# Kernel optimization log

Hardware: AMD Instinct MI355X
Metric: run time of the kernel (lower is better)

## Reference

```python
import jax, jax.numpy as jnp
import numpy as np

SCALE = 0.1  # FullAttention(0.1) binds scale positionally

def setup_inputs() -> dict:
    key = jax.random.key(0)
    k1, k2, k3, k4, k5 = jax.random.split(key, 5)
    B, H, L, E = 128, 16, 64, 128
    C = H * E  # in_channel = 2048
    return {
        "queries": jax.random.normal(k1, (B, H, L, E), dtype=jnp.float32),
        "keys": jax.random.normal(k2, (B, H, L, E), dtype=jnp.float32),
        "values": jax.random.normal(k3, (B, H, L, E), dtype=jnp.float32),
        "W": jax.random.normal(k4, (C, C), dtype=jnp.float32) * (1.0 / np.sqrt(C)),
        "b": jax.random.normal(k5, (C,), dtype=jnp.float32) * 0.01,
    }

def reference(queries, keys, values, W, b):
    # inputs are [B, H, L, E]; module permutes to [B, L, H, E]
    q = jnp.transpose(queries, (0, 2, 1, 3))  # blhe
    k = jnp.transpose(keys, (0, 2, 1, 3))     # bshe
    v = jnp.transpose(values, (0, 2, 1, 3))   # bshd
    scores = jnp.einsum('blhe,bshe->bhls', q, k)
    A = jax.nn.softmax(SCALE * scores, axis=-1)  # dropout is identity in eval
    V = jnp.einsum('bhls,bshd->blhd', A, v)
    B_, L, H, D = V.shape
    out = V.reshape(-1, 64, H * D)  # view(-1, 64, in_channel)
    return out @ W.T + b
```

## Files before the change

kernel.cpp:

```cpp
#include <hip/hip_runtime.h>
#include <hip/hip_bf16.h>
#include <stdint.h>

typedef __bf16 bf16_t;
typedef __bf16 bf16x4 __attribute__((ext_vector_type(4)));
typedef __bf16 bf16x8 __attribute__((ext_vector_type(8)));
typedef float  f32x4  __attribute__((ext_vector_type(4)));

#define AS1 __attribute__((address_space(1)))
#define AS3 __attribute__((address_space(3)))

__device__ __forceinline__ void gld_lds16(const void* gp, void* lp) {
    __builtin_amdgcn_global_load_lds((const AS1 unsigned int*)gp,
                                     (AS3 unsigned int*)lp, 16, 0, 0);
}

__device__ __forceinline__ bf16_t bhi(float v) { return (bf16_t)v; }
__device__ __forceinline__ bf16_t blo(float v) {
    return (bf16_t)(v - (float)((bf16_t)v));
}

__global__ __launch_bounds__(256) void wconv_kernel(const float* __restrict__ W,
                                                    bf16_t* __restrict__ Wb) {
    const int i = (blockIdx.x * 256 + threadIdx.x) * 4;
    const float4 f = *(const float4*)&W[i];
    bf16x4 v = { (bf16_t)f.x, (bf16_t)f.y, (bf16_t)f.z, (bf16_t)f.w };
    *(bf16x4*)&Wb[i] = v;
}

__global__ __launch_bounds__(256, 3) void attn_kernel(const float* __restrict__ Q,
                                                      const float* __restrict__ K,
                                                      const float* __restrict__ V,
                                                      bf16_t* __restrict__ X) {
    __shared__ __align__(16) char smem[49152];
    bf16_t* KL = (bf16_t*)smem;
    bf16_t* KH = (bf16_t*)(smem + 16384);
    bf16_t* Vt = (bf16_t*)(smem + 32768);
    bf16_t* Ps = (bf16_t*)smem;
    bf16_t* Ob = (bf16_t*)(smem + 16384);

    const int bh    = blockIdx.x;
    const int b     = bh >> 4;
    const int h     = bh & 15;
    const int t     = threadIdx.x;
    const int w     = t >> 6;
    const int lane  = t & 63;
    const int row16 = lane & 15;
    const int quad  = lane >> 4;

    const float* Qg = Q + (size_t)bh * 8192;
    const float* Kg = K + (size_t)bh * 8192;
    const float* Vg = V + (size_t)bh * 8192;

    bf16x8 qh8[4], ql8[4];
    {
        const float* qrow = Qg + (size_t)(16 * w + row16) * 128 + 8 * quad;
#pragma unroll
        for (int kc = 0; kc < 4; ++kc) {
            const float4 f0 = *(const float4*)&qrow[32 * kc];
            const float4 f1 = *(const float4*)&qrow[32 * kc + 4];
            const float f[8] = { f0.x, f0.y, f0.z, f0.w, f1.x, f1.y, f1.z, f1.w };
            bf16x8 hi, lo;
#pragma unroll
            for (int j = 0; j < 8; ++j) {
                const bf16_t hv = (bf16_t)f[j];
                hi[j] = hv;
                lo[j] = (bf16_t)(f[j] - (float)hv);
            }
            qh8[kc] = hi;
            ql8[kc] = lo;
        }
    }

    {
        const int r   = t >> 2;
        const int c0  = (t & 3) * 32;
        const int rsw = r & 7;
#pragma unroll
        for (int j = 0; j < 8; ++j) {
            const int c = c0 + 4 * j;
            const float4 f = *(const float4*)&Kg[r * 128 + c];
            bf16x4 hi = { bhi(f.x), bhi(f.y), bhi(f.z), bhi(f.w) };
            bf16x4 lo = { blo(f.x), blo(f.y), blo(f.z), blo(f.w) };
            const int addr = r * 128 + ((((c >> 3) ^ rsw)) << 3) + (c & 7);
            *(bf16x4*)&KH[addr] = hi;
            *(bf16x4*)&KL[addr] = lo;
        }
    }

    {
        const int s = lane;
#pragma unroll
        for (int j = 0; j < 8; ++j) {
            const int d0 = 32 * w + 4 * j;
            const float4 f = *(const float4*)&Vg[(size_t)s * 128 + d0];
            const float ff[4] = { f.x, f.y, f.z, f.w };
#pragma unroll
            for (int i = 0; i < 4; ++i) {
                const int d = d0 + i;
                Vt[d * 64 + ((((s >> 3) ^ (d & 7))) << 3) + (s & 7)] = (bf16_t)ff[i];
            }
        }
    }

    __syncthreads();

    f32x4 accS[4];
#pragma unroll
    for (int ni = 0; ni < 4; ++ni) accS[ni] = (f32x4){0.f, 0.f, 0.f, 0.f};
    const int bsw = row16 & 7;

#define SPASS(AREG, BS)                                                        \
    {                                                                          \
        _Pragma("unroll")                                                      \
        for (int kc = 0; kc < 4; ++kc) {                                       \
            const bf16x8 a = AREG[kc];                                         \
            _Pragma("unroll")                                                  \
            for (int ni = 0; ni < 4; ++ni) {                                   \
                const bf16x8 bb = *(const bf16x8*)&BS[(16 * ni + row16) * 128  \
                                       + ((((4 * kc + quad) ^ bsw)) << 3)];    \
                accS[ni] = __builtin_amdgcn_mfma_f32_16x16x32_bf16(a, bb, accS[ni], 0, 0, 0); \
            }                                                                  \
        }                                                                      \
    }

    __builtin_amdgcn_s_setprio(1);
    SPASS(qh8, KL)
    SPASS(qh8, KH)
    SPASS(ql8, KH)
    __builtin_amdgcn_s_setprio(0);

    float e[4][4];
    float inv_[4];
    const float cs = 0.1f * 1.44269504088896f;
#pragma unroll
    for (int rr = 0; rr < 4; ++rr) {
        float m = fmaxf(fmaxf(accS[0][rr], accS[1][rr]),
                        fmaxf(accS[2][rr], accS[3][rr]));
        m = fmaxf(m, __shfl_xor(m, 1));
        m = fmaxf(m, __shfl_xor(m, 2));
        m = fmaxf(m, __shfl_xor(m, 4));
        m = fmaxf(m, __shfl_xor(m, 8));
        float s0 = 0.f;
#pragma unroll
        for (int ni = 0; ni < 4; ++ni) {
            const float ev = exp2f((accS[ni][rr] - m) * cs);
            e[ni][rr] = ev;
            s0 += ev;
        }
        s0 += __shfl_xor(s0, 1);
        s0 += __shfl_xor(s0, 2);
        s0 += __shfl_xor(s0, 4);
        s0 += __shfl_xor(s0, 8);
        inv_[rr] = 1.0f / s0;
    }

    __syncthreads();

#pragma unroll
    for (int rr = 0; rr < 4; ++rr) {
        const int l   = 16 * w + 4 * quad + rr;
        const int lsw = l & 7;
#pragma unroll
        for (int ni = 0; ni < 4; ++ni) {
            const int s = 16 * ni + row16;
            Ps[l * 64 + ((((s >> 3) ^ lsw)) << 3) + (s & 7)] = (bf16_t)e[ni][rr];
        }
    }
    asm volatile("s_waitcnt lgkmcnt(0)" ::: "memory");
    __builtin_amdgcn_sched_barrier(0);

    f32x4 accO[8];
#pragma unroll
    for (int ni = 0; ni < 8; ++ni) accO[ni] = (f32x4){0.f, 0.f, 0.f, 0.f};
    __builtin_amdgcn_s_setprio(1);
#pragma unroll
    for (int kb = 0; kb < 2; ++kb) {
        const bf16x8 a = *(const bf16x8*)&Ps[(16 * w + row16) * 64
                               + ((((4 * kb + quad) ^ bsw)) << 3)];
#pragma unroll
        for (int ni = 0; ni < 8; ++ni) {
            const bf16x8 bb = *(const bf16x8*)&Vt[(16 * ni + row16) * 64
                                   + ((((4 * kb + quad) ^ bsw)) << 3)];
            accO[ni] = __builtin_amdgcn_mfma_f32_16x16x32_bf16(a, bb, accO[ni], 0, 0, 0);
        }
    }
    __builtin_amdgcn_s_setprio(0);

#pragma unroll
    for (int ni = 0; ni < 8; ++ni)
#pragma unroll
        for (int rr = 0; rr < 4; ++rr) {
            const int l = 16 * w + 4 * quad + rr;
            const int d = 16 * ni + row16;
            Ob[l * 128 + ((((d >> 3) ^ (5 * rr))) << 3) + (d & 7)] =
                (bf16_t)(accO[ni][rr] * inv_[rr]);
        }
    asm volatile("s_waitcnt lgkmcnt(0)" ::: "memory");
    __builtin_amdgcn_sched_barrier(0);

    {
        const int lr = 16 * w + (lane >> 2);
        bf16_t* Xrow = X + (size_t)b * 64 * 2048 + h * 128 + (size_t)lr * 2048;
#pragma unroll
        for (int jj = 0; jj < 4; ++jj) {
            const int c8 = (lane & 3) + 4 * jj;
            const bf16x8 v = *(const bf16x8*)&Ob[lr * 128 + ((c8 ^ (5 * (lr & 3))) << 3)];
            *(bf16x8*)&Xrow[8 * c8] = v;
        }
    }
}

__global__ __launch_bounds__(256, 4) void gemm_kernel(const bf16_t* __restrict__ X,
                                                      const bf16_t* __restrict__ Wb,
                                                      const float* __restrict__ bias,
                                                      float* __restrict__ out) {
    __shared__ bf16_t As[128 * 64];
    __shared__ bf16_t Bs[128 * 64];

    const int t    = threadIdx.x;
    const int w    = t >> 6;
    const int lane = t & 63;
    const int row16 = lane & 15;
    const int quad  = lane >> 4;
    const int m0 = blockIdx.x * 128;
    const int n0 = blockIdx.y * 128;
    const int wm = w >> 1;
    const int wn = w & 1;

    const int row8 = lane >> 3;
    const int scol = 8 * ((lane & 7) ^ (row8 & 7));
    const bf16_t* gA = X  + (size_t)(m0 + 32 * w + row8) * 2048 + scol;
    const bf16_t* gB = Wb + (size_t)(n0 + 32 * w + row8) * 2048 + scol;
    bf16_t* lA = &As[(32 * w) * 64];
    bf16_t* lB = &Bs[(32 * w) * 64];

    const int sw = row16 & 7;
    int aoff[4][2], boff[4][2];
#pragma unroll
    for (int mi = 0; mi < 4; ++mi)
#pragma unroll
        for (int kk = 0; kk < 2; ++kk) {
            const int ar = 64 * wm + 16 * mi + row16;
            const int br = 64 * wn + 16 * mi + row16;
            aoff[mi][kk] = ar * 64 + 8 * ((4 * kk + quad) ^ sw);
            boff[mi][kk] = br * 64 + 8 * ((4 * kk + quad) ^ sw);
        }

    f32x4 acc[4][4];
#pragma unroll
    for (int mi = 0; mi < 4; ++mi)
#pragma unroll
        for (int ni = 0; ni < 4; ++ni) acc[mi][ni] = (f32x4){0.f, 0.f, 0.f, 0.f};

    for (int kb = 0; kb < 32; ++kb) {
        const int k0 = kb * 64;
        __syncthreads();
#pragma unroll
        for (int i = 0; i < 4; ++i) {
            gld_lds16(gA + (size_t)(8 * i) * 2048 + k0, lA + (8 * i) * 64);
            gld_lds16(gB + (size_t)(8 * i) * 2048 + k0, lB + (8 * i) * 64);
        }
        __syncthreads();

#pragma unroll
        for (int kk = 0; kk < 2; ++kk) {
            bf16x8 a[4], bb[4];
#pragma unroll
            for (int mi = 0; mi < 4; ++mi) a[mi]  = *(const bf16x8*)&As[aoff[mi][kk]];
#pragma unroll
            for (int ni = 0; ni < 4; ++ni) bb[ni] = *(const bf16x8*)&Bs[boff[ni][kk]];
#pragma unroll
            for (int mi = 0; mi < 4; ++mi)
#pragma unroll
                for (int ni = 0; ni < 4; ++ni)
                    acc[mi][ni] = __builtin_amdgcn_mfma_f32_16x16x32_bf16(a[mi], bb[ni], acc[mi][ni], 0, 0, 0);
        }
    }

    const int nb = n0 + 64 * wn;
    float br[4];
#pragma unroll
    for (int ni = 0; ni < 4; ++ni) br[ni] = bias[nb + 16 * ni + row16];
#pragma unroll
    for (int mi = 0; mi < 4; ++mi)
#pragma unroll
        for (int ni = 0; ni < 4; ++ni)
#pragma unroll
            for (int rr = 0; rr < 4; ++rr) {
                const int m = m0 + 64 * wm + 16 * mi + 4 * quad + rr;
                const int n = nb + 16 * ni + row16;
                out[(size_t)m * 2048 + n] = acc[mi][ni][rr] + br[ni];
            }
}

extern "C" void kernel_launch(void* const* d_in, const int* in_sizes, int n_in,
                              void* d_out, int out_size, void* d_ws, size_t ws_size,
                              hipStream_t stream) {
    const float* Q    = (const float*)d_in[0];
    const float* K    = (const float*)d_in[1];
    const float* V    = (const float*)d_in[2];
    const float* W    = (const float*)d_in[3];
    const float* bias = (const float*)d_in[4];

    bf16_t* Xws = (bf16_t*)d_ws;
    bf16_t* Wb  = (bf16_t*)((char*)d_ws + (size_t)8192 * 2048 * 2);
    float*  out = (float*)d_out;

    wconv_kernel<<<4096, 256, 0, stream>>>(W, Wb);
    attn_kernel<<<2048, 256, 0, stream>>>(Q, K, V, Xws);
    gemm_kernel<<<dim3(64, 16), 256, 0, stream>>>(Xws, Wb, bias, out);
}
```

Before: 301.3 us.

## Shrink attention LDS by staging K hi/lo in one buffer

```diff
diff --git a/kernel.cpp b/kernel.cpp
--- a/kernel.cpp
+++ b/kernel.cpp
@@ -28,16 +28,14 @@
     *(bf16x4*)&Wb[i] = v;
 }
 
-__global__ __launch_bounds__(256, 3) void attn_kernel(const float* __restrict__ Q,
+__global__ __launch_bounds__(256, 5) void attn_kernel(const float* __restrict__ Q,
                                                       const float* __restrict__ K,
                                                       const float* __restrict__ V,
                                                       bf16_t* __restrict__ X) {
-    __shared__ __align__(16) char smem[49152];
-    bf16_t* KL = (bf16_t*)smem;
-    bf16_t* KH = (bf16_t*)(smem + 16384);
-    bf16_t* Vt = (bf16_t*)(smem + 32768);
+    __shared__ __align__(16) char smem[32768];
+    bf16_t* Kb = (bf16_t*)smem;
+    bf16_t* Vt = (bf16_t*)(smem + 16384);
     bf16_t* Ps = (bf16_t*)smem;
-    bf16_t* Ob = (bf16_t*)(smem + 16384);
 
     const int bh    = blockIdx.x;
     const int b     = bh >> 4;
@@ -72,34 +70,29 @@
         }
     }
 
+    const int r   = t >> 2;
+    const int c0q = (t & 3) * 4;
+    const int rsw = r & 7;
+    bf16x8 klo[4];
+    int kaddr[4];
+#pragma unroll
+    for (int jc = 0; jc < 4; ++jc)
+        kaddr[jc] = r * 128 + (((c0q + jc) ^ rsw) << 3);
     {
-        const int r   = t >> 2;
-        const int c0  = (t & 3) * 32;
-        const int rsw = r & 7;
-#pragma unroll
-        for (int j = 0; j < 8; ++j) {
-            const int c = c0 + 4 * j;
-            const float4 f = *(const float4*)&Kg[r * 128 + c];
-            bf16x4 hi = { bhi(f.x), bhi(f.y), bhi(f.z), bhi(f.w) };
-            bf16x4 lo = { blo(f.x), blo(f.y), blo(f.z), blo(f.w) };
-            const int addr = r * 128 + ((((c >> 3) ^ rsw)) << 3) + (c & 7);
-            *(bf16x4*)&KH[addr] = hi;
-            *(bf16x4*)&KL[addr] = lo;
-        }
-    }
-
-    {
-        const int s = lane;
-#pragma unroll
-        for (int j = 0; j < 8; ++j) {
-            const int d0 = 32 * w + 4 * j;
-            const float4 f = *(const float4*)&Vg[(size_t)s * 128 + d0];
-            const float ff[4] = { f.x, f.y, f.z, f.w };
-#pragma unroll
-            for (int i = 0; i < 4; ++i) {
-                const int d = d0 + i;
-                Vt[d * 64 + ((((s >> 3) ^ (d & 7))) << 3) + (s & 7)] = (bf16_t)ff[i];
+#pragma unroll
+        for (int jc = 0; jc < 4; ++jc) {
+            const float4 f0 = *(const float4*)&Kg[r * 128 + 8 * (c0q + jc)];
+            const float4 f1 = *(const float4*)&Kg[r * 128 + 8 * (c0q + jc) + 4];
+            const float f[8] = { f0.x, f0.y, f0.z, f0.w, f1.x, f1.y, f1.z, f1.w };
+            bf16x8 hi, lo;
+#pragma unroll
+            for (int j = 0; j < 8; ++j) {
+                const bf16_t hv = (bf16_t)f[j];
+                hi[j] = hv;
+                lo[j] = (bf16_t)(f[j] - (float)hv);
             }
+            *(bf16x8*)&Kb[kaddr[jc]] = hi;
+            klo[jc] = lo;
         }
     }
 
@@ -110,14 +103,14 @@
     for (int ni = 0; ni < 4; ++ni) accS[ni] = (f32x4){0.f, 0.f, 0.f, 0.f};
     const int bsw = row16 & 7;
 
-#define SPASS(AREG, BS)                                                        \
+#define SPASS(AREG)                                                            \
     {                                                                          \
         _Pragma("unroll")                                                      \
         for (int kc = 0; kc < 4; ++kc) {                                       \
             const bf16x8 a = AREG[kc];                                         \
             _Pragma("unroll")                                                  \
             for (int ni = 0; ni < 4; ++ni) {                                   \
-                const bf16x8 bb = *(const bf16x8*)&BS[(16 * ni + row16) * 128  \
+                const bf16x8 bb = *(const bf16x8*)&Kb[(16 * ni + row16) * 128  \
                                        + ((((4 * kc + quad) ^ bsw)) << 3)];    \
                 accS[ni] = __builtin_amdgcn_mfma_f32_16x16x32_bf16(a, bb, accS[ni], 0, 0, 0); \
             }                                                                  \
@@ -125,9 +118,36 @@
     }
 
     __builtin_amdgcn_s_setprio(1);
-    SPASS(qh8, KL)
-    SPASS(qh8, KH)
-    SPASS(ql8, KH)
+    SPASS(qh8)
+    SPASS(ql8)
+    __builtin_amdgcn_s_setprio(0);
+
+    __builtin_amdgcn_sched_barrier(0);
+    {
+        const int s = lane;
+#pragma unroll
+        for (int j = 0; j < 8; ++j) {
+            const int d0 = 32 * w + 4 * j;
+            const float4 f = *(const float4*)&Vg[(size_t)s * 128 + d0];
+            const float ff[4] = { f.x, f.y, f.z, f.w };
+#pragma unroll
+            for (int i = 0; i < 4; ++i) {
+                const int d = d0 + i;
+                Vt[d * 64 + ((((s >> 3) ^ (d & 7))) << 3) + (s & 7)] = (bf16_t)ff[i];
+            }
+        }
+    }
+
+    __syncthreads();
+
+#pragma unroll
+    for (int jc = 0; jc < 4; ++jc)
+        *(bf16x8*)&Kb[kaddr[jc]] = klo[jc];
+
+    __syncthreads();
+
+    __builtin_amdgcn_s_setprio(1);
+    SPASS(qh8)
     __builtin_amdgcn_s_setprio(0);
 
     float e[4][4];
@@ -187,27 +207,15 @@
     }
     __builtin_amdgcn_s_setprio(0);
 
-#pragma unroll
-    for (int ni = 0; ni < 8; ++ni)
-#pragma unroll
-        for (int rr = 0; rr < 4; ++rr) {
-            const int l = 16 * w + 4 * quad + rr;
-            const int d = 16 * ni + row16;
-            Ob[l * 128 + ((((d >> 3) ^ (5 * rr))) << 3) + (d & 7)] =
-                (bf16_t)(accO[ni][rr] * inv_[rr]);
-        }
-    asm volatile("s_waitcnt lgkmcnt(0)" ::: "memory");
-    __builtin_amdgcn_sched_barrier(0);
-
     {
-        const int lr = 16 * w + (lane >> 2);
-        bf16_t* Xrow = X + (size_t)b * 64 * 2048 + h * 128 + (size_t)lr * 2048;
-#pragma unroll
-        for (int jj = 0; jj < 4; ++jj) {
-            const int c8 = (lane & 3) + 4 * jj;
-            const bf16x8 v = *(const bf16x8*)&Ob[lr * 128 + ((c8 ^ (5 * (lr & 3))) << 3)];
-            *(bf16x8*)&Xrow[8 * c8] = v;
-        }
+        const int lbase = 16 * w + 4 * quad;
+        bf16_t* Xb = X + (size_t)b * 131072 + (size_t)h * 128;
+#pragma unroll
+        for (int ni = 0; ni < 8; ++ni)
+#pragma unroll
+            for (int rr = 0; rr < 4; ++rr)
+                Xb[(size_t)(lbase + rr) * 2048 + 16 * ni + row16] =
+                    (bf16_t)(accO[ni][rr] * inv_[rr]);
     }
 }
 
```

Result: slower. 331.3 us (+10.0%).
